# Optimization experiments

Hardware: AMD Instinct MI355X
Metric: run time of the kernel (lower is better)

## Reference

```python
import jax, jax.numpy as jnp
import numpy as np

PC_RANGE = (-140.8, -40.0, -3.0, 140.8, 40.0, 1.0)
VOX = (0.4, 0.4, 4.0)
H_GRID = 200   # (40 - (-40)) / 0.4
W_GRID = 704   # (140.8 - (-140.8)) / 0.4
C = 256        # embed_dim
N_BOX = 128
BN_EPS = 1e-5


def _make_boxes(key, n):
    # Realistic CCW-ordered 3D box corners (bottom 4 first, matching pred_box[:, :4, :2]).
    k1, k2, k3, k4, k5 = jax.random.split(key, 5)
    cx = jax.random.uniform(k1, (n,), minval=PC_RANGE[0] + 10.0, maxval=PC_RANGE[3] - 10.0)
    cy = jax.random.uniform(k2, (n,), minval=PC_RANGE[1] + 5.0, maxval=PC_RANGE[4] - 5.0)
    L = jax.random.uniform(k3, (n,), minval=2.0, maxval=8.0)
    Wd = jax.random.uniform(k4, (n,), minval=1.0, maxval=3.0)
    yaw = jax.random.uniform(k5, (n,), minval=0.0, maxval=2.0 * np.pi)
    # CCW offsets: (+l,+w), (-l,+w), (-l,-w), (+l,-w)
    ox = jnp.stack([L, -L, -L, L], axis=1) * 0.5   # [n,4]
    oy = jnp.stack([Wd, Wd, -Wd, -Wd], axis=1) * 0.5
    c, s = jnp.cos(yaw)[:, None], jnp.sin(yaw)[:, None]
    px = c * ox - s * oy + cx[:, None]
    py = s * ox + c * oy + cy[:, None]
    bot = jnp.stack([px, py, jnp.full_like(px, -1.0)], axis=-1)  # [n,4,3]
    top = jnp.stack([px, py, jnp.full_like(px, 1.0)], axis=-1)
    return jnp.concatenate([bot, top], axis=1)  # [n,8,3]


def setup_inputs() -> dict:
    key = jax.random.key(0)
    ks = jax.random.split(key, 16)
    inp = {
        "pred_box": _make_boxes(ks[0], N_BOX),
        "pred_score": jax.random.uniform(ks[1], (N_BOX,)),
        # MLP: Linear(25,C) -> ReLU -> Linear(C,C) -> ReLU -> Linear(C,C)
        "w1": jax.random.normal(ks[2], (25, C)) * 0.1,
        "b1": jnp.zeros((C,)),
        "w2": jax.random.normal(ks[3], (C, C)) * 0.05,
        "b2": jnp.zeros((C,)),
        "w3": jax.random.normal(ks[4], (C, C)) * 0.05,
        "b3": jnp.zeros((C,)),
        # 3 refine blocks x 2 convs, OIHW
        "conv_w": jax.random.normal(ks[5], (3, 2, C, C, 3, 3)) * 0.02,
        "bn_gamma": 1.0 + 0.1 * jax.random.normal(ks[6], (3, 2, C)),
        "bn_beta": 0.1 * jax.random.normal(ks[7], (3, 2, C)),
        "bn_mean": 0.1 * jax.random.normal(ks[8], (3, 2, C)),
        "bn_var": jax.random.uniform(ks[9], (3, 2, C), minval=0.5, maxval=1.5),
    }
    return inp


def _conv(x, w):
    return jax.lax.conv_general_dilated(
        x, w, window_strides=(1, 1), padding="SAME",
        dimension_numbers=("NCHW", "OIHW", "NCHW"))


def _bn(x, g, b, m, v):
    inv = g / jnp.sqrt(v + BN_EPS)
    return x * inv[None, :, None, None] + (b - m * inv)[None, :, None, None]


def reference(pred_box, pred_score, w1, b1, w2, b2, w3, b3,
              conv_w, bn_gamma, bn_beta, bn_mean, bn_var):
    n = pred_box.shape[0]
    # per-box feature: MLP(corners flattened + score) * score
    feat = jnp.concatenate([pred_box.reshape(n, -1), pred_score[:, None]], axis=1)  # [N,25]
    h = jax.nn.relu(feat @ w1 + b1)
    h = jax.nn.relu(h @ w2 + b2)
    obj = (h @ w3 + b3) * pred_score[:, None]  # [N,C]

    xmin, ymin = PC_RANGE[0], PC_RANGE[1]
    dx, dy = VOX[0], VOX[1]
    gx = (pred_box[:, :4, 0] - xmin) / dx  # [N,4] polygon verts in grid units
    gy = (pred_box[:, :4, 1] - ymin) / dy
    cxs = jnp.arange(W_GRID, dtype=pred_box.dtype) + 0.5  # cell centers
    cys = jnp.arange(H_GRID, dtype=pred_box.dtype) + 0.5

    # point-in-quad via 4 edge cross products (all >= 0 for CCW polygon)
    inside = jnp.ones((n, H_GRID, W_GRID), dtype=bool)
    for e in range(4):
        ax, ay = gx[:, e], gy[:, e]
        bx, by = gx[:, (e + 1) % 4], gy[:, (e + 1) % 4]
        vx, vy = bx - ax, by - ay
        c = (vx[:, None, None] * (cys[None, :, None] - ay[:, None, None])
             - vy[:, None, None] * (cxs[None, None, :] - ax[:, None, None]))  # [N,H,W]
        inside = inside & (c >= 0)
    insf = inside.astype(obj.dtype)

    feat_sum = jnp.einsum("nhw,nc->chw", insf, obj)        # masked scatter-add
    feat_cnt = jnp.maximum(insf.sum(axis=0), 1.0)           # [H,W]
    x = (feat_sum / feat_cnt[None])[None]                   # [1,C,H,W]

    for blk in range(3):
        res = x
        y = jax.nn.relu(_bn(_conv(x, conv_w[blk, 0]),
                            bn_gamma[blk, 0], bn_beta[blk, 0], bn_mean[blk, 0], bn_var[blk, 0]))
        y = _bn(_conv(y, conv_w[blk, 1]),
                bn_gamma[blk, 1], bn_beta[blk, 1], bn_mean[blk, 1], bn_var[blk, 1])
        x = jax.nn.relu(y + res)
    return x[0]  # [C,H,W]
```

## Files before the change

kernel.cpp:

```cpp
#include <hip/hip_runtime.h>

#define HG 200
#define WGR 704
#define CC 256
#define NBOX 128

typedef unsigned short u16;
typedef __attribute__((ext_vector_type(8))) short short8;
typedef __attribute__((ext_vector_type(4))) short short4v;
typedef __attribute__((ext_vector_type(4))) float floatx4;

typedef __attribute__((address_space(1))) const unsigned int guint;
typedef __attribute__((address_space(3))) unsigned int luint;

__device__ __forceinline__ float bf2f(u16 u) {
  unsigned int x = ((unsigned int)u) << 16;
  return __builtin_bit_cast(float, x);
}
__device__ __forceinline__ u16 f2bf(float f) {
  unsigned int x = __builtin_bit_cast(unsigned int, f);
  x += 0x7fffu + ((x >> 16) & 1u);
  return (u16)(x >> 16);
}

__global__ __launch_bounds__(256) void pack_w_kernel(const float* __restrict__ cw, u16* __restrict__ W2) {
  int i = blockIdx.x * 256 + threadIdx.x;
  int conv = i / 589824;
  int r = i - conv * 589824;
  int tap = r / 65536;
  int r2 = r - tap * 65536;
  int ck = r2 >> 13;
  int r3 = r2 & 8191;
  int cogrp = r3 >> 9;
  int r4 = r3 & 511;
  int lane = r4 >> 3;
  int j = r4 & 7;
  int co = cogrp * 16 + (lane & 15);
  int ci = ck * 32 + (lane >> 4) * 8 + j;
  W2[i] = f2bf(cw[((conv * 256 + co) * 256 + ci) * 9 + tap]);
}

__global__ __launch_bounds__(256) void bn_prep_kernel(const float* __restrict__ g, const float* __restrict__ b,
                                                      const float* __restrict__ m, const float* __restrict__ v,
                                                      float* __restrict__ binv, float* __restrict__ bbias) {
  int i = blockIdx.x * 256 + threadIdx.x;
  float inv = g[i] / sqrtf(v[i] + 1e-5f);
  binv[i] = inv;
  bbias[i] = b[i] - m[i] * inv;
}

__global__ __launch_bounds__(128) void box_prep_kernel(const float* __restrict__ pb, float* __restrict__ geo) {
  int b = threadIdx.x;
  float gx[4], gy[4];
#pragma unroll
  for (int j = 0; j < 4; ++j) {
    float px = pb[(b * 8 + j) * 3 + 0];
    float py = pb[(b * 8 + j) * 3 + 1];
    gx[j] = __fdiv_rn(__fsub_rn(px, -140.8f), 0.4f);
    gy[j] = __fdiv_rn(__fsub_rn(py, -40.0f), 0.4f);
  }
  float* g = geo + b * 16;
#pragma unroll
  for (int e = 0; e < 4; ++e) {
    g[e * 4 + 0] = gx[e];
    g[e * 4 + 1] = gy[e];
    g[e * 4 + 2] = __fsub_rn(gx[(e + 1) & 3], gx[e]);
    g[e * 4 + 3] = __fsub_rn(gy[(e + 1) & 3], gy[e]);
  }
}

__global__ __launch_bounds__(256) void mlp_kernel(
    const float* __restrict__ pb, const float* __restrict__ score,
    const float* __restrict__ w1, const float* __restrict__ b1,
    const float* __restrict__ w2, const float* __restrict__ b2,
    const float* __restrict__ w3, const float* __restrict__ b3,
    float* __restrict__ obj) {
  __shared__ float sf[25];
  __shared__ float h1[256];
  __shared__ float h2[256];
  int b = blockIdx.x, t = threadIdx.x;
  if (t < 24) sf[t] = pb[b * 24 + t];
  if (t == 24) sf[24] = score[b];
  __syncthreads();
  float a = b1[t];
  for (int k = 0; k < 25; ++k) a += sf[k] * w1[k * 256 + t];
  h1[t] = fmaxf(a, 0.0f);
  __syncthreads();
  a = b2[t];
  for (int k = 0; k < 256; ++k) a += h1[k] * w2[k * 256 + t];
  h2[t] = fmaxf(a, 0.0f);
  __syncthreads();
  a = b3[t];
  for (int k = 0; k < 256; ++k) a += h2[k] * w3[k * 256 + t];
  obj[b * 256 + t] = a * score[b];
}

__global__ __launch_bounds__(256) void raster_kernel(
    const float* __restrict__ geo, const float* __restrict__ obj, u16* __restrict__ x0) {
  __shared__ float sG[NBOX * 17];
  int tid = threadIdx.x;
  for (int i = tid; i < NBOX * 16; i += 256) sG[(i >> 4) * 17 + (i & 15)] = geo[i];
  __syncthreads();
  int wid = tid >> 6, lane = tid & 63;
  int cell = blockIdx.x * 4 + wid;
  int h = cell / WGR, w = cell - h * WGR;
  float cx = w + 0.5f, cy = h + 0.5f;

  auto test = [&](int n) -> bool {
    const float* g = &sG[n * 17];
    bool ok = true;
#pragma unroll
    for (int e = 0; e < 4; ++e) {
      float ax = g[e * 4 + 0], ay = g[e * 4 + 1];
      float vx = g[e * 4 + 2], vy = g[e * 4 + 3];
      float c = __fsub_rn(__fmul_rn(vx, __fsub_rn(cy, ay)),
                          __fmul_rn(vy, __fsub_rn(cx, ax)));
      ok = ok && (c >= 0.0f);
    }
    return ok;
  };

  unsigned long long m0 = __ballot(test(lane));
  unsigned long long m1 = __ballot(test(lane + 64));
  int cnt = __popcll(m0) + __popcll(m1);
  floatx4 s = {0.f, 0.f, 0.f, 0.f};
  while (m0) { int n = __builtin_ctzll(m0); m0 &= m0 - 1; s += *(const floatx4*)(obj + n * CC + lane * 4); }
  while (m1) { int n = 64 + __builtin_ctzll(m1); m1 &= m1 - 1; s += *(const floatx4*)(obj + n * CC + lane * 4); }
  float cf = fmaxf((float)cnt, 1.0f);
  short4v o;
#pragma unroll
  for (int j = 0; j < 4; ++j) o[j] = (short)f2bf(__fdiv_rn(s[j], cf));
  *(short4v*)(x0 + cell * CC + lane * 4) = o;
}

template <bool ADD_RES>
__global__ __launch_bounds__(256, 2) void conv_kernel(
    const u16* __restrict__ in, const u16* __restrict__ wgt,
    const float* __restrict__ bninv, const float* __restrict__ bnbias,
    const u16* __restrict__ res, u16* __restrict__ out) {
  __shared__ u16 sA[2 * 1584 * 8];

  const int w0 = blockIdx.x * 64;
  const int h0 = blockIdx.y * 4;
  const int c0g = blockIdx.z * 8;
  const int tid = threadIdx.x;
  const int lane = tid & 63;
  const int wid = tid >> 6;
  const int ln15 = lane & 15;
  const int quad = lane >> 4;
  const int rp = wid >> 1;
  const int ni = wid & 1;

  const u16* ga[7];
  bool gv[7];
#pragma unroll
  for (int j = 0; j < 7; ++j) {
    int I = wid + 4 * j;
    int s = I * 64 + lane;
    int r = s / 264;
    int rem = s - r * 264;
    int q = rem / 66;
    int px = rem - q * 66;
    int gh = h0 + r - 1;
    int gw = w0 + px - 1;
    bool ok = (I <= 24) && (s < 1584) &&
              ((unsigned)gh < (unsigned)HG) && ((unsigned)gw < (unsigned)WGR);
    ga[j] = in + (gh * WGR + gw) * CC + q * 8;
    gv[j] = ok;
    if (I <= 24 && s < 1584 && !ok) {
      short8 z = {};
      *(short8*)(&sA[s * 8]) = z;
      *(short8*)(&sA[(1584 + s) * 8]) = z;
    }
  }

  auto dma = [&](int buf) {
#pragma unroll
    for (int j = 0; j < 7; ++j) {
      int I = wid + 4 * j;
      if (I <= 24) {
        u16* lp = &sA[buf * 12672 + I * 512];
        if (gv[j])
          __builtin_amdgcn_global_load_lds((guint*)(const void*)ga[j], (luint*)(void*)lp, 16, 0, 0);
      }
      ga[j] += 32;
    }
  };

  const u16* wbase = wgt + ((size_t)(c0g + ni * 4)) * 512 + lane * 8;
  auto loadB = [&](int ck, int tap, short8* dst) {
#pragma unroll
    for (int nt = 0; nt < 4; ++nt)
      dst[nt] = *(const short8*)(wbase + ((tap * 8 + ck) * 16 + nt) * 512);
  };

  floatx4 acc0[4][4] = {};
  floatx4 acc1[4][4] = {};
  short8 A0[4], A1[4];
  short8 B[2][4];
  dma(0);

  for (int ck = 0; ck < 8; ++ck) {
    const int cur = ck & 1;
    __syncthreads();
    loadB(ck, 0, B[0]);
    loadB(ck, 1, B[1]);
    if (ck < 7) dma(1 - cur);

    const u16* base = &sA[cur * 12672];
#pragma unroll
    for (int mt = 0; mt < 4; ++mt)
      A0[mt] = *(const short8*)(base + (((rp * 2) * 4 + quad) * 66 + mt * 16 + ln15) * 8);

#pragma unroll
    for (int t = 0; t < 9; ++t) {
      const int kh = t / 3;
      const int kw = t - kh * 3;
#pragma unroll
      for (int mt = 0; mt < 4; ++mt)
        A1[mt] = *(const short8*)(base + (((rp * 2 + 1 + kh) * 4 + quad) * 66 + mt * 16 + ln15 + kw) * 8);
      __builtin_amdgcn_s_setprio(1);
#pragma unroll
      for (int mt = 0; mt < 4; ++mt)
#pragma unroll
        for (int nt = 0; nt < 4; ++nt)
          acc0[mt][nt] = __builtin_amdgcn_mfma_f32_16x16x32_bf16(A0[mt], B[t & 1][nt], acc0[mt][nt], 0, 0, 0);
      __builtin_amdgcn_s_setprio(0);
      if (t < 8) {
        const int kh2 = (t + 1) / 3;
        const int kw2 = (t + 1) - kh2 * 3;
#pragma unroll
        for (int mt = 0; mt < 4; ++mt)
          A0[mt] = *(const short8*)(base + (((rp * 2 + kh2) * 4 + quad) * 66 + mt * 16 + ln15 + kw2) * 8);
      }
      __builtin_amdgcn_s_setprio(1);
#pragma unroll
      for (int mt = 0; mt < 4; ++mt)
#pragma unroll
        for (int nt = 0; nt < 4; ++nt)
          acc1[mt][nt] = __builtin_amdgcn_mfma_f32_16x16x32_bf16(A1[mt], B[t & 1][nt], acc1[mt][nt], 0, 0, 0);
      __builtin_amdgcn_s_setprio(0);
      if (t < 7) loadB(ck, t + 2, B[t & 1]);
    }
  }

  float binv[4], bbia[4];
#pragma unroll
  for (int nt = 0; nt < 4; ++nt) {
    int co = (c0g + ni * 4 + nt) * 16 + ln15;
    binv[nt] = bninv[co];
    bbia[nt] = bnbias[co];
  }

#pragma unroll
  for (int rr = 0; rr < 2; ++rr) {
    const int h = h0 + rp * 2 + rr;
#pragma unroll
    for (int mt = 0; mt < 4; ++mt) {
#pragma unroll
      for (int nt = 0; nt < 4; ++nt) {
        int co = (c0g + ni * 4 + nt) * 16 + ln15;
#pragma unroll
        for (int r = 0; r < 4; ++r) {
          int w = w0 + mt * 16 + quad * 4 + r;
          int idx = (h * WGR + w) * CC + co;
          float v = (rr ? acc1[mt][nt][r] : acc0[mt][nt][r]) * binv[nt] + bbia[nt];
          if (ADD_RES) v += bf2f(res[idx]);
          v = fmaxf(v, 0.0f);
          out[idx] = f2bf(v);
        }
      }
    }
  }
}

__global__ __launch_bounds__(256) void transpose_kernel(const u16* __restrict__ src, float* __restrict__ dst) {
  __shared__ u16 sT[64][68];
  int w0 = blockIdx.x * 64, h = blockIdx.y, c0 = blockIdx.z * 64;
  int tid = threadIdx.x;
  int cl = (tid & 15) * 4, wl = tid >> 4;
#pragma unroll
  for (int i = 0; i < 4; ++i) {
    int w = wl + i * 16;
    short4v v = *(const short4v*)(src + (h * WGR + w0 + w) * CC + c0 + cl);
    *(short4v*)(&sT[w][cl]) = v;
  }
  __syncthreads();
  int w4 = (tid & 15) * 4, ch = tid >> 4;
#pragma unroll
  for (int i = 0; i < 4; ++i) {
    int c = ch + i * 16;
    floatx4 v;
    v[0] = bf2f(sT[w4 + 0][c]);
    v[1] = bf2f(sT[w4 + 1][c]);
    v[2] = bf2f(sT[w4 + 2][c]);
    v[3] = bf2f(sT[w4 + 3][c]);
    *(floatx4*)(dst + (size_t)(c0 + c) * (HG * WGR) + h * WGR + w0 + w4) = v;
  }
}

extern "C" void kernel_launch(void* const* d_in, const int* in_sizes, int n_in,
                              void* d_out, int out_size, void* d_ws, size_t ws_size,
                              hipStream_t stream) {
  const float* pred_box = (const float*)d_in[0];
  const float* pred_score = (const float*)d_in[1];
  const float* w1 = (const float*)d_in[2];
  const float* b1 = (const float*)d_in[3];
  const float* w2 = (const float*)d_in[4];
  const float* b2 = (const float*)d_in[5];
  const float* w3 = (const float*)d_in[6];
  const float* b3 = (const float*)d_in[7];
  const float* conv_w = (const float*)d_in[8];
  const float* bng = (const float*)d_in[9];
  const float* bnb = (const float*)d_in[10];
  const float* bnm = (const float*)d_in[11];
  const float* bnv = (const float*)d_in[12];

  char* ws = (char*)d_ws;
  u16* W2       = (u16*)(ws);
  u16* Abuf     = (u16*)(ws + 7077888);
  float* obj    = (float*)(ws + 79167488);
  float* bninv  = (float*)(ws + 79298560);
  float* bnbias = (float*)(ws + 79304704);
  float* geo    = (float*)(ws + 79310848);
  u16* SCR = (u16*)d_out;
  float* OUT = (float*)d_out;

  pack_w_kernel<<<13824, 256, 0, stream>>>(conv_w, W2);
  bn_prep_kernel<<<6, 256, 0, stream>>>(bng, bnb, bnm, bnv, bninv, bnbias);
  box_prep_kernel<<<1, 128, 0, stream>>>(pred_box, geo);
  mlp_kernel<<<NBOX, 256, 0, stream>>>(pred_box, pred_score, w1, b1, w2, b2, w3, b3, obj);
  raster_kernel<<<35200, 256, 0, stream>>>(geo, obj, Abuf);

  dim3 cg(11, 50, 2);
  conv_kernel<false><<<cg, 256, 0, stream>>>(Abuf, W2 + 0 * 589824, bninv + 0 * 256, bnbias + 0 * 256, nullptr, SCR);
  conv_kernel<true ><<<cg, 256, 0, stream>>>(SCR,  W2 + 1 * 589824, bninv + 1 * 256, bnbias + 1 * 256, Abuf, Abuf);
  conv_kernel<false><<<cg, 256, 0, stream>>>(Abuf, W2 + 2 * 589824, bninv + 2 * 256, bnbias + 2 * 256, nullptr, SCR);
  conv_kernel<true ><<<cg, 256, 0, stream>>>(SCR,  W2 + 3 * 589824, bninv + 3 * 256, bnbias + 3 * 256, Abuf, Abuf);
  conv_kernel<false><<<cg, 256, 0, stream>>>(Abuf, W2 + 4 * 589824, bninv + 4 * 256, bnbias + 4 * 256, nullptr, SCR);
  conv_kernel<true ><<<cg, 256, 0, stream>>>(SCR,  W2 + 5 * 589824, bninv + 5 * 256, bnbias + 5 * 256, Abuf, Abuf);
  transpose_kernel<<<dim3(11, HG, 4), 256, 0, stream>>>(Abuf, OUT);
}
```

Before: 1.080 ms.

## Split conv work across 8 waves, one output row per wave

The conv kernel moves from 4 waves, each computing two output rows, to 8 waves per block, each computing one output row. This halves the accumulator and A-fragment registers per wave and sets launch bounds to 512 threads with 4 blocks, so more waves can be resident to hide LDS and global latency. In exchange, each B weight fragment loaded from global memory now feeds half as many MFMAs, and the reuse of A rows between kernel-row taps across adjacent output rows is lost. That raises weight traffic per unit of compute.

```diff
diff --git a/kernel.cpp b/kernel.cpp
--- a/kernel.cpp
+++ b/kernel.cpp
@@ -134,7 +134,7 @@
 }
 
 template <bool ADD_RES>
-__global__ __launch_bounds__(256, 2) void conv_kernel(
+__global__ __launch_bounds__(512, 4) void conv_kernel(
     const u16* __restrict__ in, const u16* __restrict__ wgt,
     const float* __restrict__ bninv, const float* __restrict__ bnbias,
     const u16* __restrict__ res, u16* __restrict__ out) {
@@ -148,14 +148,14 @@
   const int wid = tid >> 6;
   const int ln15 = lane & 15;
   const int quad = lane >> 4;
-  const int rp = wid >> 1;
+  const int mi = wid >> 1;
   const int ni = wid & 1;
 
-  const u16* ga[7];
-  bool gv[7];
-#pragma unroll
-  for (int j = 0; j < 7; ++j) {
-    int I = wid + 4 * j;
+  const u16* ga[4];
+  bool gv[4];
+#pragma unroll
+  for (int j = 0; j < 4; ++j) {
+    int I = wid + 8 * j;
     int s = I * 64 + lane;
     int r = s / 264;
     int rem = s - r * 264;
@@ -176,8 +176,8 @@
 
   auto dma = [&](int buf) {
 #pragma unroll
-    for (int j = 0; j < 7; ++j) {
-      int I = wid + 4 * j;
+    for (int j = 0; j < 4; ++j) {
+      int I = wid + 8 * j;
       if (I <= 24) {
         u16* lp = &sA[buf * 12672 + I * 512];
         if (gv[j])
@@ -194,9 +194,8 @@
       dst[nt] = *(const short8*)(wbase + ((tap * 8 + ck) * 16 + nt) * 512);
   };
 
-  floatx4 acc0[4][4] = {};
-  floatx4 acc1[4][4] = {};
-  short8 A0[4], A1[4];
+  floatx4 acc[4][4] = {};
+  short8 A[4];
   short8 B[2][4];
   dma(0);
 
@@ -210,36 +209,24 @@
     const u16* base = &sA[cur * 12672];
 #pragma unroll
     for (int mt = 0; mt < 4; ++mt)
-      A0[mt] = *(const short8*)(base + (((rp * 2) * 4 + quad) * 66 + mt * 16 + ln15) * 8);
+      A[mt] = *(const short8*)(base + ((mi * 4 + quad) * 66 + mt * 16 + ln15) * 8);
 
 #pragma unroll
     for (int t = 0; t < 9; ++t) {
-      const int kh = t / 3;
-      const int kw = t - kh * 3;
+      __builtin_amdgcn_s_setprio(1);
 #pragma unroll
       for (int mt = 0; mt < 4; ++mt)
-        A1[mt] = *(const short8*)(base + (((rp * 2 + 1 + kh) * 4 + quad) * 66 + mt * 16 + ln15 + kw) * 8);
-      __builtin_amdgcn_s_setprio(1);
-#pragma unroll
-      for (int mt = 0; mt < 4; ++mt)
 #pragma unroll
         for (int nt = 0; nt < 4; ++nt)
-          acc0[mt][nt] = __builtin_amdgcn_mfma_f32_16x16x32_bf16(A0[mt], B[t & 1][nt], acc0[mt][nt], 0, 0, 0);
+          acc[mt][nt] = __builtin_amdgcn_mfma_f32_16x16x32_bf16(A[mt], B[t & 1][nt], acc[mt][nt], 0, 0, 0);
       __builtin_amdgcn_s_setprio(0);
       if (t < 8) {
         const int kh2 = (t + 1) / 3;
         const int kw2 = (t + 1) - kh2 * 3;
 #pragma unroll
         for (int mt = 0; mt < 4; ++mt)
-          A0[mt] = *(const short8*)(base + (((rp * 2 + kh2) * 4 + quad) * 66 + mt * 16 + ln15 + kw2) * 8);
+          A[mt] = *(const short8*)(base + (((mi + kh2) * 4 + quad) * 66 + mt * 16 + ln15 + kw2) * 8);
       }
-      __builtin_amdgcn_s_setprio(1);
-#pragma unroll
-      for (int mt = 0; mt < 4; ++mt)
-#pragma unroll
-        for (int nt = 0; nt < 4; ++nt)
-          acc1[mt][nt] = __builtin_amdgcn_mfma_f32_16x16x32_bf16(A1[mt], B[t & 1][nt], acc1[mt][nt], 0, 0, 0);
-      __builtin_amdgcn_s_setprio(0);
       if (t < 7) loadB(ck, t + 2, B[t & 1]);
     }
   }
@@ -252,23 +239,20 @@
     bbia[nt] = bnbias[co];
   }
 
-#pragma unroll
-  for (int rr = 0; rr < 2; ++rr) {
-    const int h = h0 + rp * 2 + rr;
-#pragma unroll
-    for (int mt = 0; mt < 4; ++mt) {
-#pragma unroll
-      for (int nt = 0; nt < 4; ++nt) {
-        int co = (c0g + ni * 4 + nt) * 16 + ln15;
-#pragma unroll
-        for (int r = 0; r < 4; ++r) {
-          int w = w0 + mt * 16 + quad * 4 + r;
-          int idx = (h * WGR + w) * CC + co;
-          float v = (rr ? acc1[mt][nt][r] : acc0[mt][nt][r]) * binv[nt] + bbia[nt];
-          if (ADD_RES) v += bf2f(res[idx]);
-          v = fmaxf(v, 0.0f);
-          out[idx] = f2bf(v);
-        }
+  const int h = h0 + mi;
+#pragma unroll
+  for (int mt = 0; mt < 4; ++mt) {
+#pragma unroll
+    for (int nt = 0; nt < 4; ++nt) {
+      int co = (c0g + ni * 4 + nt) * 16 + ln15;
+#pragma unroll
+      for (int r = 0; r < 4; ++r) {
+        int w = w0 + mt * 16 + quad * 4 + r;
+        int idx = (h * WGR + w) * CC + co;
+        float v = acc[mt][nt][r] * binv[nt] + bbia[nt];
+        if (ADD_RES) v += bf2f(res[idx]);
+        v = fmaxf(v, 0.0f);
+        out[idx] = f2bf(v);
       }
     }
   }
@@ -333,11 +317,11 @@
   raster_kernel<<<35200, 256, 0, stream>>>(geo, obj, Abuf);
 
   dim3 cg(11, 50, 2);
-  conv_kernel<false><<<cg, 256, 0, stream>>>(Abuf, W2 + 0 * 589824, bninv + 0 * 256, bnbias + 0 * 256, nullptr, SCR);
-  conv_kernel<true ><<<cg, 256, 0, stream>>>(SCR,  W2 + 1 * 589824, bninv + 1 * 256, bnbias + 1 * 256, Abuf, Abuf);
-  conv_kernel<false><<<cg, 256, 0, stream>>>(Abuf, W2 + 2 * 589824, bninv + 2 * 256, bnbias + 2 * 256, nullptr, SCR);
-  conv_kernel<true ><<<cg, 256, 0, stream>>>(SCR,  W2 + 3 * 589824, bninv + 3 * 256, bnbias + 3 * 256, Abuf, Abuf);
-  conv_kernel<false><<<cg, 256, 0, stream>>>(Abuf, W2 + 4 * 589824, bninv + 4 * 256, bnbias + 4 * 256, nullptr, SCR);
-  conv_kernel<true ><<<cg, 256, 0, stream>>>(SCR,  W2 + 5 * 589824, bninv + 5 * 256, bnbias + 5 * 256, Abuf, Abuf);
+  conv_kernel<false><<<cg, 512, 0, stream>>>(Abuf, W2 + 0 * 589824, bninv + 0 * 256, bnbias + 0 * 256, nullptr, SCR);
+  conv_kernel<true ><<<cg, 512, 0, stream>>>(SCR,  W2 + 1 * 589824, bninv + 1 * 256, bnbias + 1 * 256, Abuf, Abuf);
+  conv_kernel<false><<<cg, 512, 0, stream>>>(Abuf, W2 + 2 * 589824, bninv + 2 * 256, bnbias + 2 * 256, nullptr, SCR);
+  conv_kernel<true ><<<cg, 512, 0, stream>>>(SCR,  W2 + 3 * 589824, bninv + 3 * 256, bnbias + 3 * 256, Abuf, Abuf);
+  conv_kernel<false><<<cg, 512, 0, stream>>>(Abuf, W2 + 4 * 589824, bninv + 4 * 256, bnbias + 4 * 256, nullptr, SCR);
+  conv_kernel<true ><<<cg, 512, 0, stream>>>(SCR,  W2 + 5 * 589824, bninv + 5 * 256, bnbias + 5 * 256, Abuf, Abuf);
   transpose_kernel<<<dim3(11, HG, 4), 256, 0, stream>>>(Abuf, OUT);
 }
```

Result: slower. 1.306 ms (+20.9%).
